# Optimization experiments

Measured on AMD Instinct MI355X. Metric: run time of the kernel, lower is better.

The kernel has to match this reference:

```python
import jax, jax.numpy as jnp
import numpy as np

T, D, N, H = 2032, 1408, 16, 88  # K == N (MHA vision attention)
BLOCK_SIZE = 128
ROPE_THETA = 10000.0


def _apply_rope_interleaved(x_tnh, freqs_cis):
    # x_tnh: [T, N, H]; freqs_cis: [T, H//2, 2] with (..., 0)=cos, (..., 1)=sin.
    cos = freqs_cis[:, None, :, 0]  # [T, 1, H//2]
    sin = freqs_cis[:, None, :, 1]
    x1 = x_tnh[..., 0::2]
    x2 = x_tnh[..., 1::2]
    # interleaved rotation: pairs (even, odd) rotated by angle theta_t
    rot = jnp.stack([x1 * cos - x2 * sin, x1 * sin + x2 * cos], axis=-1)
    return rot.reshape(x_tnh.shape)


def setup_inputs() -> dict:
    key = jax.random.key(0)
    ks = jax.random.split(key, 10)
    s = 0.02
    x = jax.random.normal(ks[0], (T, D), dtype=jnp.float32)
    # precomputed rotary cos/sin table (interleaved ordering)
    pos = jnp.arange(T, dtype=jnp.float32)
    inv_freq = ROPE_THETA ** (-jnp.arange(0, H, 2, dtype=jnp.float32) / H)  # [H//2]
    ang = pos[:, None] * inv_freq[None, :]                                  # [T, H//2]
    freqs_cis = jnp.stack([jnp.cos(ang), jnp.sin(ang)], axis=-1)            # [T, H//2, 2]
    Wq = jax.random.normal(ks[1], (D, N, H), dtype=jnp.float32) * s
    Wk = jax.random.normal(ks[2], (D, N, H), dtype=jnp.float32) * s
    Wv = jax.random.normal(ks[3], (D, N, H), dtype=jnp.float32) * s
    Wo = jax.random.normal(ks[4], (N, H, D), dtype=jnp.float32) * s
    bq = jax.random.normal(ks[5], (N, H), dtype=jnp.float32) * s
    bk = jax.random.normal(ks[6], (N, H), dtype=jnp.float32) * s
    bv = jax.random.normal(ks[7], (N, H), dtype=jnp.float32) * s
    bo = jax.random.normal(ks[8], (D,), dtype=jnp.float32) * s
    return {"x": x, "freqs_cis": freqs_cis, "Wq": Wq, "bq": bq, "Wk": Wk,
            "bk": bk, "Wv": Wv, "bv": bv, "Wo": Wo, "bo": bo}


def reference(x, freqs_cis, Wq, bq, Wk, bk, Wv, bv, Wo, bo):
    t, d = x.shape
    n, h = bq.shape
    sm_scale = h ** -0.5
    # fused QKV projections + bias + RoPE (q, k only)
    q = jnp.einsum('td,dnh->tnh', x, Wq) + bq[None]
    q = _apply_rope_interleaved(q, freqs_cis)
    k = jnp.einsum('td,dkh->tkh', x, Wk) + bk[None]
    k = _apply_rope_interleaved(k, freqs_cis)
    v = jnp.einsum('td,dkh->tkh', x, Wv) + bv[None]
    # pad T up to a multiple of BLOCK_SIZE, as the flash-attention call requires
    pad_len = (BLOCK_SIZE - t % BLOCK_SIZE) % BLOCK_SIZE
    qp = jnp.pad(q, ((0, pad_len), (0, 0), (0, 0)))
    kp = jnp.pad(k, ((0, pad_len), (0, 0), (0, 0)))
    vp = jnp.pad(v, ((0, pad_len), (0, 0), (0, 0)))
    # [N, Tp, H]
    qh = jnp.transpose(qp, (1, 0, 2))
    kh = jnp.transpose(kp, (1, 0, 2))
    vh = jnp.transpose(vp, (1, 0, 2))
    # segment ids: 0 for valid tokens, 1 for padding; attention only within equal ids
    seg = jnp.concatenate([jnp.zeros((t,), jnp.int32), jnp.ones((pad_len,), jnp.int32)])
    mask = seg[:, None] == seg[None, :]  # [Tp, Tp]
    scores = jnp.einsum('nth,nsh->nts', qh, kh) * sm_scale
    scores = jnp.where(mask[None], scores, jnp.finfo(scores.dtype).min)
    probs = jax.nn.softmax(scores, axis=-1)
    out = jnp.einsum('nts,nsh->nth', probs, vh)        # [N, Tp, H]
    out = jnp.transpose(out, (1, 0, 2))[:t]            # [T, N, H]
    o = jnp.einsum('tnh,nhd->td', out, Wo) + bo
    return o
```

## Files before the change

### kernel.cpp

```cpp
#include <hip/hip_runtime.h>
#include <hip/hip_bf16.h>
#include <stdint.h>
#include <stddef.h>

typedef __bf16 bf16_t;
typedef __bf16 bf16x8 __attribute__((ext_vector_type(8)));
typedef __bf16 bf16x4 __attribute__((ext_vector_type(4)));
typedef float  f32x4  __attribute__((ext_vector_type(4)));

#define T_SEQ 2032
#define T_PAD 2048
#define DM    1408
#define NHEAD 16
#define HD    88
#define HPQ   96
#define HPK   128
#define HPV   96
#define KVB   64
#define NT    (T_PAD / KVB)
#define SM_SCALE 0.10660035817780521f

__device__ __forceinline__ void gload_lds16(const bf16_t* g, bf16_t* l) {
  __builtin_amdgcn_global_load_lds(
      (__attribute__((address_space(1))) void*)(g),
      (__attribute__((address_space(3))) void*)(l), 16, 0, 0);
}

__global__ void k_convert_x(const float* __restrict__ x, bf16_t* __restrict__ Xb) {
  int idx = blockIdx.x * 256 + threadIdx.x;
  const int total = T_PAD * DM / 4;
  if (idx >= total) return;
  int base = idx * 4;
  int t = base / DM;
  float4 v;
  if (t < T_SEQ) v = *(const float4*)(x + base);
  else           v = make_float4(0.f, 0.f, 0.f, 0.f);
  bf16x4 o;
  o[0] = (bf16_t)v.x; o[1] = (bf16_t)v.y; o[2] = (bf16_t)v.z; o[3] = (bf16_t)v.w;
  *(bf16x4*)(Xb + base) = o;
}

__device__ __forceinline__ void transpose_body(const float* __restrict__ src,
                                               bf16_t* __restrict__ dst,
                                               int R, int C, int blk) {
  __shared__ float tile[32][33];
  const int tiles_c = C >> 5;
  const int tr = blk / tiles_c;
  const int tc = blk % tiles_c;
  const int lane = threadIdx.x & 31;
  const int row  = threadIdx.x >> 5;
#pragma unroll
  for (int i = 0; i < 32; i += 8)
    tile[row + i][lane] = src[(size_t)(tr * 32 + row + i) * C + tc * 32 + lane];
  __syncthreads();
#pragma unroll
  for (int i = 0; i < 32; i += 8)
    dst[(size_t)(tc * 32 + row + i) * R + tr * 32 + lane] = (bf16_t)tile[lane][row + i];
}

__global__ void k_transpose3(const float* __restrict__ Wq, const float* __restrict__ Wk,
                             const float* __restrict__ Wv, bf16_t* __restrict__ dst) {
  const int which = blockIdx.x / 1936;
  const int b = blockIdx.x % 1936;
  const float* src = (which == 0) ? Wq : (which == 1) ? Wk : Wv;
  transpose_body(src, dst + (size_t)which * DM * DM, DM, DM, b);
}

__global__ void k_transpose1(const float* __restrict__ src, bf16_t* __restrict__ dst) {
  transpose_body(src, dst, DM, DM, blockIdx.x);
}

__global__ void k_bias(const float* __restrict__ bq, const float* __restrict__ bk,
                       const float* __restrict__ bv, float* __restrict__ bias) {
  int i = blockIdx.x * 256 + threadIdx.x;
  if (i >= 3 * DM) return;
  bias[i] = (i < DM) ? bq[i] : ((i < 2 * DM) ? bk[i - DM] : bv[i - 2 * DM]);
}

__device__ __forceinline__ void gemm_main_1408(
    const bf16_t* __restrict__ A, const bf16_t* __restrict__ Bt,
    bf16_t* As, bf16_t* Bs, int m0, int n0, f32x4 acc[4][4]) {
  const int tid = threadIdx.x;
  const int w = tid >> 6, lane = tid & 63;
  const int l15 = lane & 15, lg = lane >> 4;
  const int b0 = w * 2048 + lane * 16;
  const int r0 = b0 >> 6, k0 = (b0 & 63) >> 1;
  const int b1 = b0 + 1024;
  const int r1 = b1 >> 6, k1 = (b1 & 63) >> 1;
  const int wr = w >> 1, wc = w & 1;
  const size_t aoff0 = (size_t)(m0 + r0) * DM + k0;
  const size_t aoff1 = (size_t)(m0 + r1) * DM + k1;
  const size_t boff0 = (size_t)(n0 + r0) * DM + k0;
  const size_t boff1 = (size_t)(n0 + r1) * DM + k1;
  for (int kt = 0; kt < 44; ++kt) {
    const int ko = kt * 32;
    gload_lds16(A + aoff0 + ko, As + w * 1024);
    gload_lds16(A + aoff1 + ko, As + w * 1024 + 512);
    gload_lds16(Bt + boff0 + ko, Bs + w * 1024);
    gload_lds16(Bt + boff1 + ko, Bs + w * 1024 + 512);
    __syncthreads();
    bf16x8 av[4], bv[4];
#pragma unroll
    for (int m = 0; m < 4; ++m)
      av[m] = *(const bf16x8*)(As + (wr * 64 + m * 16 + l15) * 32 + lg * 8);
#pragma unroll
    for (int n = 0; n < 4; ++n)
      bv[n] = *(const bf16x8*)(Bs + (wc * 64 + n * 16 + l15) * 32 + lg * 8);
#pragma unroll
    for (int m = 0; m < 4; ++m)
#pragma unroll
      for (int n = 0; n < 4; ++n)
        acc[m][n] = __builtin_amdgcn_mfma_f32_16x16x32_bf16(av[m], bv[n], acc[m][n], 0, 0, 0);
    __syncthreads();
  }
}

__global__ __launch_bounds__(256, 2) void k_gemm_qkv(
    const bf16_t* __restrict__ A, const bf16_t* __restrict__ Bt,
    const float* __restrict__ bias, const float* __restrict__ freqs,
    bf16_t* __restrict__ Qh, bf16_t* __restrict__ Kh, bf16_t* __restrict__ Vt) {
  __shared__ bf16_t As[128 * 32];
  __shared__ bf16_t Bs[128 * 32];
  const int bid = blockIdx.x;
  const int sbid = (bid & 7) * 66 + (bid >> 3);
  const int mt = sbid / 33, nt = sbid % 33;
  f32x4 acc[4][4];
#pragma unroll
  for (int m = 0; m < 4; ++m)
#pragma unroll
    for (int n = 0; n < 4; ++n) acc[m][n] = (f32x4){0.f, 0.f, 0.f, 0.f};
  gemm_main_1408(A, Bt, As, Bs, mt * 128, nt * 128, acc);
  const int tid = threadIdx.x, w = tid >> 6, lane = tid & 63;
  const int l15 = lane & 15, lg = lane >> 4;
  const int wr = w >> 1, wc = w & 1;
  const int cb = nt * 128 + wc * 64, rb = mt * 128 + wr * 64;
#pragma unroll
  for (int n = 0; n < 4; ++n) {
    const int col = cb + n * 16 + l15;
    const float bv = bias[col];
    const int seg = (col >= 2 * DM) ? 2 : ((col >= DM) ? 1 : 0);
    const int cc = col - seg * DM;
    const int hn = cc / 88;
    const int hh = cc - hn * 88;
    const int hbase = hh & ~1;
    const bool odd = hh & 1;
#pragma unroll
    for (int m = 0; m < 4; ++m) {
      const int tb = rb + m * 16 + lg * 4;
      if (seg == 2) {
        bf16x4 vv;
#pragma unroll
        for (int r = 0; r < 4; ++r) vv[r] = (bf16_t)(acc[m][n][r] + bv);
        *(bf16x4*)(Vt + ((size_t)hn * HPV + hh) * T_PAD + tb) = vv;
      } else {
#pragma unroll
        for (int r = 0; r < 4; ++r) {
          const int t = tb + r;
          const float v = acc[m][n][r] + bv;
          const float p = __shfl_xor(v, 1);
          const int tc2 = (t < T_SEQ) ? t : 0;
          const float c = freqs[tc2 * 88 + hbase];
          const float s = freqs[tc2 * 88 + hbase + 1];
          const float x1 = odd ? p : v;
          const float x2 = odd ? v : p;
          const float ro = odd ? (x1 * s + x2 * c) : (x1 * c - x2 * s);
          if (seg == 0)
            Qh[((size_t)hn * T_PAD + t) * HPQ + hh] = (bf16_t)(ro * SM_SCALE);
          else
            Kh[((size_t)hn * T_PAD + t) * HPK + hh] = (bf16_t)ro;
        }
      }
    }
  }
}

__global__ __launch_bounds__(256, 2) void k_gemm_out64(
    const bf16_t* __restrict__ A, const bf16_t* __restrict__ Bt,
    const float* __restrict__ bo, float* __restrict__ out) {
  __shared__ bf16_t Sm[6144];
  const int bid = blockIdx.x;
  const int sbid = (bid & 7) * 44 + (bid >> 3);
  const int mt = sbid / 11, nt = sbid % 11;
  const int m0 = mt * 64, n0 = nt * 128;
  const int tid = threadIdx.x, w = tid >> 6, lane = tid & 63;
  const int l15 = lane & 15, lg = lane >> 4;
  const bf16_t* srcp[3];
  size_t srco[3];
  int dste[3];
#pragma unroll
  for (int p = 0; p < 3; ++p) {
    const int off = w * 3072 + p * 1024;
    const int o = off + lane * 16;
    dste[p] = off >> 1;
    if (off < 4096) {
      int r = o >> 6, k = (o & 63) >> 1;
      srcp[p] = A; srco[p] = (size_t)(m0 + r) * DM + k;
    } else {
      int ob = o - 4096;
      int r = ob >> 6, k = (ob & 63) >> 1;
      srcp[p] = Bt; srco[p] = (size_t)(n0 + r) * DM + k;
    }
  }
  f32x4 acc[4][2];
#pragma unroll
  for (int m = 0; m < 4; ++m)
#pragma unroll
    for (int n = 0; n < 2; ++n) acc[m][n] = (f32x4){0.f, 0.f, 0.f, 0.f};
  for (int kt = 0; kt < 44; ++kt) {
    const int ko = kt * 32;
#pragma unroll
    for (int p = 0; p < 3; ++p)
      gload_lds16(srcp[p] + srco[p] + ko, Sm + dste[p]);
    __syncthreads();
    bf16x8 av[4], bv2[2];
#pragma unroll
    for (int m = 0; m < 4; ++m)
      av[m] = *(const bf16x8*)(Sm + (m * 16 + l15) * 32 + lg * 8);
#pragma unroll
    for (int n = 0; n < 2; ++n)
      bv2[n] = *(const bf16x8*)(Sm + 2048 + (w * 32 + n * 16 + l15) * 32 + lg * 8);
#pragma unroll
    for (int m = 0; m < 4; ++m)
#pragma unroll
      for (int n = 0; n < 2; ++n)
        acc[m][n] = __builtin_amdgcn_mfma_f32_16x16x32_bf16(av[m], bv2[n], acc[m][n], 0, 0, 0);
    __syncthreads();
  }
  const int cb = n0 + w * 32;
#pragma unroll
  for (int n = 0; n < 2; ++n) {
    const int col = cb + n * 16 + l15;
    const float bv = bo[col];
#pragma unroll
    for (int m = 0; m < 4; ++m) {
#pragma unroll
      for (int r = 0; r < 4; ++r) {
        const int t = m0 + m * 16 + lg * 4 + r;
        if (t < T_SEQ) out[(size_t)t * DM + col] = acc[m][n][r] + bv;
      }
    }
  }
}

__global__ __launch_bounds__(256, 3) void k_attn(
    const bf16_t* __restrict__ Qh, const bf16_t* __restrict__ Kh,
    const bf16_t* __restrict__ Vt, bf16_t* __restrict__ Ob) {
  __shared__ bf16_t Ks[2][KVB * 128];
  __shared__ bf16_t Vs[HPV * KVB];
  __shared__ bf16_t Ps[4][16 * 72];
  const int tid = threadIdx.x;
  const int w = tid >> 6, lane = tid & 63;
  const int l15 = lane & 15, lg = lane >> 4;
  const int swz = l15 & 7;
  const int bid = blockIdx.x;
  const int sbid = (bid & 7) * 64 + (bid >> 3);
  const int head = sbid >> 5;
  const int qt = sbid & 31;
  const bf16_t* Qn = Qh + (size_t)head * T_PAD * HPQ;
  const bf16_t* Kn = Kh + (size_t)head * T_PAD * HPK;
  const bf16_t* Vn = Vt + (size_t)head * HPV * T_PAD;
  const int q0 = qt * 64 + w * 16;

  bf16x8 qf[3];
#pragma unroll
  for (int kh = 0; kh < 3; ++kh)
    qf[kh] = *(const bf16x8*)(Qn + (size_t)(q0 + l15) * HPQ + kh * 32 + lg * 8);

  f32x4 oacc[6];
#pragma unroll
  for (int j = 0; j < 6; ++j) oacc[j] = (f32x4){0.f, 0.f, 0.f, 0.f};
  float mrow[4] = {-1e30f, -1e30f, -1e30f, -1e30f};
  float lrowp[4] = {0.f, 0.f, 0.f, 0.f};

  int kro[4], kco[4];
#pragma unroll
  for (int p = 0; p < 4; ++p) {
    int o = (w * 4 + p) * 1024 + lane * 16;
    int row = o >> 8, ch = (o >> 4) & 15;
    kro[p] = row; kco[p] = (ch ^ (row & 7)) << 3;
  }
  int vro[3], vco[3];
#pragma unroll
  for (int p = 0; p < 3; ++p) {
    int o = (w * 3 + p) * 1024 + lane * 16;
    int row = o >> 7, ch = (o >> 4) & 7;
    vro[p] = row; vco[p] = (ch ^ (row & 7)) << 3;
  }

#pragma unroll
  for (int p = 0; p < 4; ++p)
    gload_lds16(Kn + (size_t)kro[p] * HPK + kco[p], &Ks[0][(w * 4 + p) * 512]);
#pragma unroll
  for (int p = 0; p < 3; ++p)
    gload_lds16(Vn + (size_t)vro[p] * T_PAD + vco[p], &Vs[(w * 3 + p) * 512]);

  for (int kvt = 0; kvt < NT; ++kvt) {
    const int s0 = kvt * KVB;
    const int cur = kvt & 1;
    const int nxt = (kvt + 1 < NT) ? kvt + 1 : 0;
#pragma unroll
    for (int p = 0; p < 4; ++p)
      gload_lds16(Kn + (size_t)(nxt * KVB + kro[p]) * HPK + kco[p],
                  &Ks[cur ^ 1][(w * 4 + p) * 512]);
    asm volatile("s_waitcnt vmcnt(4)" ::: "memory");
    __builtin_amdgcn_s_barrier();

    const bf16_t* Kc = Ks[cur];
    f32x4 sf[4];
    __builtin_amdgcn_s_setprio(1);
#pragma unroll
    for (int ss = 0; ss < 4; ++ss) {
      const int rowK = ss * 16 + l15;
      f32x4 s = {0.f, 0.f, 0.f, 0.f};
#pragma unroll
      for (int kh = 0; kh < 3; ++kh) {
        bf16x8 kf = *(const bf16x8*)(Kc + rowK * 128 + (((kh * 4 + lg) ^ swz) << 3));
        s = __builtin_amdgcn_mfma_f32_16x16x32_bf16(qf[kh], kf, s, 0, 0, 0);
      }
      if (s0 + rowK >= T_SEQ) s = (f32x4){-1e30f, -1e30f, -1e30f, -1e30f};
      sf[ss] = s;
    }
    __builtin_amdgcn_s_setprio(0);
    float tm[4];
#pragma unroll
    for (int r = 0; r < 4; ++r)
      tm[r] = fmaxf(fmaxf(sf[0][r], sf[1][r]), fmaxf(sf[2][r], sf[3][r]));
#pragma unroll
    for (int d = 1; d < 16; d <<= 1)
#pragma unroll
      for (int r = 0; r < 4; ++r) tm[r] = fmaxf(tm[r], __shfl_xor(tm[r], d, 16));
    float sc[4];
#pragma unroll
    for (int r = 0; r < 4; ++r) {
      float mn = fmaxf(mrow[r], tm[r]);
      sc[r] = __expf(mrow[r] - mn);
      mrow[r] = mn;
    }
#pragma unroll
    for (int r = 0; r < 4; ++r) {
      float rs = 0.f;
#pragma unroll
      for (int ss = 0; ss < 4; ++ss) {
        float p = __expf(sf[ss][r] - mrow[r]);
        sf[ss][r] = p;
        rs += p;
      }
      lrowp[r] = lrowp[r] * sc[r] + rs;
    }
#pragma unroll
    for (int j = 0; j < 6; ++j)
#pragma unroll
      for (int r = 0; r < 4; ++r) oacc[j][r] *= sc[r];
#pragma unroll
    for (int ss = 0; ss < 4; ++ss)
#pragma unroll
      for (int r = 0; r < 4; ++r)
        Ps[w][(lg * 4 + r) * 72 + ss * 16 + l15] = (bf16_t)sf[ss][r];
    bf16x8 pa[2];
#pragma unroll
    for (int ks = 0; ks < 2; ++ks)
      pa[ks] = *(const bf16x8*)(&Ps[w][l15 * 72 + ks * 32 + lg * 8]);
    __builtin_amdgcn_s_setprio(1);
#pragma unroll
    for (int j = 0; j < 6; ++j)
#pragma unroll
      for (int ks = 0; ks < 2; ++ks) {
        bf16x8 vf = *(const bf16x8*)(Vs + (j * 16 + l15) * KVB + (((ks * 4 + lg) ^ swz) << 3));
        oacc[j] = __builtin_amdgcn_mfma_f32_16x16x32_bf16(pa[ks], vf, oacc[j], 0, 0, 0);
      }
    __builtin_amdgcn_s_setprio(0);
    __builtin_amdgcn_s_barrier();
#pragma unroll
    for (int p = 0; p < 3; ++p)
      gload_lds16(Vn + (size_t)vro[p] * T_PAD + nxt * KVB + vco[p],
                  &Vs[(w * 3 + p) * 512]);
  }
  asm volatile("s_waitcnt vmcnt(0)" ::: "memory");

#pragma unroll
  for (int d = 1; d < 16; d <<= 1)
#pragma unroll
    for (int r = 0; r < 4; ++r) lrowp[r] += __shfl_xor(lrowp[r], d, 16);

#pragma unroll
  for (int j = 0; j < 6; ++j) {
    const int h = j * 16 + l15;
    if (h < HD) {
#pragma unroll
      for (int r = 0; r < 4; ++r) {
        const int t = q0 + lg * 4 + r;
        if (t < T_SEQ)
          Ob[(size_t)t * DM + head * HD + h] = (bf16_t)(oacc[j][r] / lrowp[r]);
      }
    }
  }
}

extern "C" void kernel_launch(void* const* d_in, const int* in_sizes, int n_in,
                              void* d_out, int out_size, void* d_ws, size_t ws_size,
                              hipStream_t stream) {
  (void)in_sizes; (void)n_in; (void)out_size; (void)ws_size;
  const float* x     = (const float*)d_in[0];
  const float* freqs = (const float*)d_in[1];
  const float* Wq    = (const float*)d_in[2];
  const float* bq    = (const float*)d_in[3];
  const float* Wk    = (const float*)d_in[4];
  const float* bk    = (const float*)d_in[5];
  const float* Wv    = (const float*)d_in[6];
  const float* bv    = (const float*)d_in[7];
  const float* Wo    = (const float*)d_in[8];
  const float* bo    = (const float*)d_in[9];
  float* out = (float*)d_out;
  char* ws = (char*)d_ws;

  bf16_t* Xb   = (bf16_t*)(ws);
  bf16_t* Wt   = (bf16_t*)(ws + 5767168);
  float*  bias = (float*) (ws + 17661952);
  bf16_t* Qh   = (bf16_t*)(ws + 17678848);
  bf16_t* Kh   = (bf16_t*)(ws + 23970304);
  bf16_t* Vt   = (bf16_t*)(ws + 32358912);
  bf16_t* Ob   = Xb;
  bf16_t* Wot  = Wt;

  hipMemsetAsync(Qh, 0, 14680064, stream);

  k_convert_x<<<(T_PAD * DM / 4 + 255) / 256, 256, 0, stream>>>(x, Xb);
  k_transpose3<<<3 * 1936, 256, 0, stream>>>(Wq, Wk, Wv, Wt);
  k_bias<<<17, 256, 0, stream>>>(bq, bk, bv, bias);

  k_gemm_qkv<<<16 * 33, 256, 0, stream>>>(Xb, Wt, bias, freqs, Qh, Kh, Vt);

  k_transpose1<<<1936, 256, 0, stream>>>(Wo, Wot);

  k_attn<<<NHEAD * 32, 256, 0, stream>>>(Qh, Kh, Vt, Ob);
  k_gemm_out64<<<32 * 11, 256, 0, stream>>>(Ob, Wot, bo, out);
}
```

Before: 256.5 us.

## Double-buffer GEMMs, merge weight transposes, rework attention with deferred rescale

The three Wq/Wk/Wv transposes and the Wo transpose are merged into one kernel that uses 64x64 float4 tiles, and the separate bias-concat kernel is dropped. Both GEMMs now double-buffer their LDS tiles, prefetching the next K-slice before computing the current one and raising wave priority around the MFMAs. Attention is restructured: the score tile is computed transposed as K·Q with KV blocks of 128, and K/V are read straight from global memory instead of staged through LDS. Softmax uses exp2, with log2e folded into the Q scale, and skips the running-max rescale unless the max grows past a threshold. These changes add register pressure and move all K/V reuse onto the caches, and the Wo placement now depends on the workspace size.

```diff
diff --git a/kernel.cpp b/kernel.cpp
--- a/kernel.cpp
+++ b/kernel.cpp
@@ -13,12 +13,12 @@
 #define DM    1408
 #define NHEAD 16
 #define HD    88
-#define HPQ   96
-#define HPK   128
-#define HPV   96
-#define KVB   64
+#define HP    96
+#define KVB   128
 #define NT    (T_PAD / KVB)
 #define SM_SCALE 0.10660035817780521f
+#define LOG2E 1.4426950408889634f
+#define DEFER_THR 8.0f
 
 __device__ __forceinline__ void gload_lds16(const bf16_t* g, bf16_t* l) {
   __builtin_amdgcn_global_load_lds(
@@ -40,46 +40,38 @@
   *(bf16x4*)(Xb + base) = o;
 }
 
-__device__ __forceinline__ void transpose_body(const float* __restrict__ src,
-                                               bf16_t* __restrict__ dst,
-                                               int R, int C, int blk) {
-  __shared__ float tile[32][33];
-  const int tiles_c = C >> 5;
-  const int tr = blk / tiles_c;
-  const int tc = blk % tiles_c;
-  const int lane = threadIdx.x & 31;
-  const int row  = threadIdx.x >> 5;
-#pragma unroll
-  for (int i = 0; i < 32; i += 8)
-    tile[row + i][lane] = src[(size_t)(tr * 32 + row + i) * C + tc * 32 + lane];
+__global__ void k_transpose4(const float* __restrict__ W0, const float* __restrict__ W1,
+                             const float* __restrict__ W2, const float* __restrict__ W3,
+                             bf16_t* __restrict__ d012, bf16_t* __restrict__ d3) {
+  const int which = blockIdx.x / 484;
+  const int b = blockIdx.x % 484;
+  const float* src = (which == 0) ? W0 : (which == 1) ? W1 : (which == 2) ? W2 : W3;
+  bf16_t* dst = (which < 3) ? (d012 + (size_t)which * DM * DM) : d3;
+  const int tr = b / 22, tc = b % 22;
+  __shared__ float tile[64][65];
+  const int t = threadIdx.x;
+  const int row = t >> 2, l4 = t & 3;
+#pragma unroll
+  for (int i = 0; i < 4; ++i) {
+    float4 v = *(const float4*)(src + (size_t)(tr * 64 + row) * DM + tc * 64 + l4 * 16 + i * 4);
+    *(float4*)&tile[row][l4 * 16 + i * 4] = v;
+  }
   __syncthreads();
-#pragma unroll
-  for (int i = 0; i < 32; i += 8)
-    dst[(size_t)(tc * 32 + row + i) * R + tr * 32 + lane] = (bf16_t)tile[lane][row + i];
-}
-
-__global__ void k_transpose3(const float* __restrict__ Wq, const float* __restrict__ Wk,
-                             const float* __restrict__ Wv, bf16_t* __restrict__ dst) {
-  const int which = blockIdx.x / 1936;
-  const int b = blockIdx.x % 1936;
-  const float* src = (which == 0) ? Wq : (which == 1) ? Wk : Wv;
-  transpose_body(src, dst + (size_t)which * DM * DM, DM, DM, b);
-}
-
-__global__ void k_transpose1(const float* __restrict__ src, bf16_t* __restrict__ dst) {
-  transpose_body(src, dst, DM, DM, blockIdx.x);
-}
-
-__global__ void k_bias(const float* __restrict__ bq, const float* __restrict__ bk,
-                       const float* __restrict__ bv, float* __restrict__ bias) {
-  int i = blockIdx.x * 256 + threadIdx.x;
-  if (i >= 3 * DM) return;
-  bias[i] = (i < DM) ? bq[i] : ((i < 2 * DM) ? bk[i - DM] : bv[i - 2 * DM]);
+  const int jj = t >> 2;
+#pragma unroll
+  for (int it = 0; it < 2; ++it) {
+    const int c = (t & 3) + 4 * it;
+    bf16x8 o;
+#pragma unroll
+    for (int e = 0; e < 8; ++e) o[e] = (bf16_t)tile[c * 8 + e][jj];
+    *(bf16x8*)(dst + (size_t)(tc * 64 + jj) * DM + tr * 64 + c * 8) = o;
+  }
 }
 
 __device__ __forceinline__ void gemm_main_1408(
     const bf16_t* __restrict__ A, const bf16_t* __restrict__ Bt,
-    bf16_t* As, bf16_t* Bs, int m0, int n0, f32x4 acc[4][4]) {
+    bf16_t* As, bf16_t* Bs,
+    int m0, int n0, f32x4 acc[4][4]) {
   const int tid = threadIdx.x;
   const int w = tid >> 6, lane = tid & 63;
   const int l15 = lane & 15, lg = lane >> 4;
@@ -92,35 +84,48 @@
   const size_t aoff1 = (size_t)(m0 + r1) * DM + k1;
   const size_t boff0 = (size_t)(n0 + r0) * DM + k0;
   const size_t boff1 = (size_t)(n0 + r1) * DM + k1;
+  gload_lds16(A + aoff0, As + w * 1024);
+  gload_lds16(A + aoff1, As + w * 1024 + 512);
+  gload_lds16(Bt + boff0, Bs + w * 1024);
+  gload_lds16(Bt + boff1, Bs + w * 1024 + 512);
   for (int kt = 0; kt < 44; ++kt) {
-    const int ko = kt * 32;
-    gload_lds16(A + aoff0 + ko, As + w * 1024);
-    gload_lds16(A + aoff1 + ko, As + w * 1024 + 512);
-    gload_lds16(Bt + boff0 + ko, Bs + w * 1024);
-    gload_lds16(Bt + boff1 + ko, Bs + w * 1024 + 512);
-    __syncthreads();
+    const int cur = kt & 1;
+    const int kon = ((kt < 43) ? kt + 1 : 43) * 32;
+    const int db = (cur ^ 1) * 4096;
+    gload_lds16(A + aoff0 + kon, As + db + w * 1024);
+    gload_lds16(A + aoff1 + kon, As + db + w * 1024 + 512);
+    gload_lds16(Bt + boff0 + kon, Bs + db + w * 1024);
+    gload_lds16(Bt + boff1 + kon, Bs + db + w * 1024 + 512);
+    asm volatile("s_waitcnt vmcnt(4)" ::: "memory");
+    __builtin_amdgcn_s_barrier();
+    const bf16_t* Ac = As + cur * 4096;
+    const bf16_t* Bc = Bs + cur * 4096;
     bf16x8 av[4], bv[4];
 #pragma unroll
     for (int m = 0; m < 4; ++m)
-      av[m] = *(const bf16x8*)(As + (wr * 64 + m * 16 + l15) * 32 + lg * 8);
+      av[m] = *(const bf16x8*)(Ac + (wr * 64 + m * 16 + l15) * 32 + lg * 8);
 #pragma unroll
     for (int n = 0; n < 4; ++n)
-      bv[n] = *(const bf16x8*)(Bs + (wc * 64 + n * 16 + l15) * 32 + lg * 8);
+      bv[n] = *(const bf16x8*)(Bc + (wc * 64 + n * 16 + l15) * 32 + lg * 8);
+    __builtin_amdgcn_s_setprio(1);
 #pragma unroll
     for (int m = 0; m < 4; ++m)
 #pragma unroll
       for (int n = 0; n < 4; ++n)
         acc[m][n] = __builtin_amdgcn_mfma_f32_16x16x32_bf16(av[m], bv[n], acc[m][n], 0, 0, 0);
-    __syncthreads();
-  }
+    __builtin_amdgcn_s_setprio(0);
+    __builtin_amdgcn_s_barrier();
+  }
+  asm volatile("s_waitcnt vmcnt(0)" ::: "memory");
 }
 
 __global__ __launch_bounds__(256, 2) void k_gemm_qkv(
     const bf16_t* __restrict__ A, const bf16_t* __restrict__ Bt,
-    const float* __restrict__ bias, const float* __restrict__ freqs,
+    const float* __restrict__ bq, const float* __restrict__ bk,
+    const float* __restrict__ bvp, const float* __restrict__ freqs,
     bf16_t* __restrict__ Qh, bf16_t* __restrict__ Kh, bf16_t* __restrict__ Vt) {
-  __shared__ bf16_t As[128 * 32];
-  __shared__ bf16_t Bs[128 * 32];
+  __shared__ bf16_t As[2 * 4096];
+  __shared__ bf16_t Bs[2 * 4096];
   const int bid = blockIdx.x;
   const int sbid = (bid & 7) * 66 + (bid >> 3);
   const int mt = sbid / 33, nt = sbid % 33;
@@ -137,9 +142,10 @@
 #pragma unroll
   for (int n = 0; n < 4; ++n) {
     const int col = cb + n * 16 + l15;
-    const float bv = bias[col];
     const int seg = (col >= 2 * DM) ? 2 : ((col >= DM) ? 1 : 0);
     const int cc = col - seg * DM;
+    const float* bp = (seg == 0) ? bq : (seg == 1) ? bk : bvp;
+    const float bval = bp[cc];
     const int hn = cc / 88;
     const int hh = cc - hn * 88;
     const int hbase = hh & ~1;
@@ -150,13 +156,13 @@
       if (seg == 2) {
         bf16x4 vv;
 #pragma unroll
-        for (int r = 0; r < 4; ++r) vv[r] = (bf16_t)(acc[m][n][r] + bv);
-        *(bf16x4*)(Vt + ((size_t)hn * HPV + hh) * T_PAD + tb) = vv;
+        for (int r = 0; r < 4; ++r) vv[r] = (bf16_t)(acc[m][n][r] + bval);
+        *(bf16x4*)(Vt + ((size_t)hn * HP + hh) * T_PAD + tb) = vv;
       } else {
 #pragma unroll
         for (int r = 0; r < 4; ++r) {
           const int t = tb + r;
-          const float v = acc[m][n][r] + bv;
+          const float v = acc[m][n][r] + bval;
           const float p = __shfl_xor(v, 1);
           const int tc2 = (t < T_SEQ) ? t : 0;
           const float c = freqs[tc2 * 88 + hbase];
@@ -165,9 +171,9 @@
           const float x2 = odd ? v : p;
           const float ro = odd ? (x1 * s + x2 * c) : (x1 * c - x2 * s);
           if (seg == 0)
-            Qh[((size_t)hn * T_PAD + t) * HPQ + hh] = (bf16_t)(ro * SM_SCALE);
+            Qh[((size_t)hn * T_PAD + t) * HP + hh] = (bf16_t)(ro * (SM_SCALE * LOG2E));
           else
-            Kh[((size_t)hn * T_PAD + t) * HPK + hh] = (bf16_t)ro;
+            Kh[((size_t)hn * T_PAD + t) * HP + hh] = (bf16_t)ro;
         }
       }
     }
@@ -177,7 +183,7 @@
 __global__ __launch_bounds__(256, 2) void k_gemm_out64(
     const bf16_t* __restrict__ A, const bf16_t* __restrict__ Bt,
     const float* __restrict__ bo, float* __restrict__ out) {
-  __shared__ bf16_t Sm[6144];
+  __shared__ bf16_t Sm[2 * 6144];
   const int bid = blockIdx.x;
   const int sbid = (bid & 7) * 44 + (bid >> 3);
   const int mt = sbid / 11, nt = sbid % 11;
@@ -206,182 +212,173 @@
   for (int m = 0; m < 4; ++m)
 #pragma unroll
     for (int n = 0; n < 2; ++n) acc[m][n] = (f32x4){0.f, 0.f, 0.f, 0.f};
+#pragma unroll
+  for (int p = 0; p < 3; ++p) gload_lds16(srcp[p] + srco[p], Sm + dste[p]);
   for (int kt = 0; kt < 44; ++kt) {
-    const int ko = kt * 32;
+    const int cur = kt & 1;
+    const int kon = ((kt < 43) ? kt + 1 : 43) * 32;
+    const int db = (cur ^ 1) * 6144;
 #pragma unroll
     for (int p = 0; p < 3; ++p)
-      gload_lds16(srcp[p] + srco[p] + ko, Sm + dste[p]);
-    __syncthreads();
+      gload_lds16(srcp[p] + srco[p] + kon, Sm + db + dste[p]);
+    asm volatile("s_waitcnt vmcnt(3)" ::: "memory");
+    __builtin_amdgcn_s_barrier();
+    const bf16_t* Sc = Sm + cur * 6144;
     bf16x8 av[4], bv2[2];
 #pragma unroll
     for (int m = 0; m < 4; ++m)
-      av[m] = *(const bf16x8*)(Sm + (m * 16 + l15) * 32 + lg * 8);
+      av[m] = *(const bf16x8*)(Sc + (m * 16 + l15) * 32 + lg * 8);
 #pragma unroll
     for (int n = 0; n < 2; ++n)
-      bv2[n] = *(const bf16x8*)(Sm + 2048 + (w * 32 + n * 16 + l15) * 32 + lg * 8);
+      bv2[n] = *(const bf16x8*)(Sc + 2048 + (w * 32 + n * 16 + l15) * 32 + lg * 8);
+    __builtin_amdgcn_s_setprio(1);
 #pragma unroll
     for (int m = 0; m < 4; ++m)
 #pragma unroll
       for (int n = 0; n < 2; ++n)
         acc[m][n] = __builtin_amdgcn_mfma_f32_16x16x32_bf16(av[m], bv2[n], acc[m][n], 0, 0, 0);
-    __syncthreads();
-  }
+    __builtin_amdgcn_s_setprio(0);
+    __builtin_amdgcn_s_barrier();
+  }
+  asm volatile("s_waitcnt vmcnt(0)" ::: "memory");
   const int cb = n0 + w * 32;
 #pragma unroll
   for (int n = 0; n < 2; ++n) {
     const int col = cb + n * 16 + l15;
-    const float bv = bo[col];
+    const float bval = bo[col];
 #pragma unroll
     for (int m = 0; m < 4; ++m) {
 #pragma unroll
       for (int r = 0; r < 4; ++r) {
         const int t = m0 + m * 16 + lg * 4 + r;
-        if (t < T_SEQ) out[(size_t)t * DM + col] = acc[m][n][r] + bv;
-      }
-    }
-  }
-}
-
-__global__ __launch_bounds__(256, 3) void k_attn(
+        if (t < T_SEQ) out[(size_t)t * DM + col] = acc[m][n][r] + bval;
+      }
+    }
+  }
+}
+
+__global__ __launch_bounds__(256, 2) void k_attn(
     const bf16_t* __restrict__ Qh, const bf16_t* __restrict__ Kh,
     const bf16_t* __restrict__ Vt, bf16_t* __restrict__ Ob) {
-  __shared__ bf16_t Ks[2][KVB * 128];
-  __shared__ bf16_t Vs[HPV * KVB];
-  __shared__ bf16_t Ps[4][16 * 72];
+  __shared__ bf16_t Ps[4][16 * 136];
   const int tid = threadIdx.x;
   const int w = tid >> 6, lane = tid & 63;
   const int l15 = lane & 15, lg = lane >> 4;
-  const int swz = l15 & 7;
   const int bid = blockIdx.x;
   const int sbid = (bid & 7) * 64 + (bid >> 3);
   const int head = sbid >> 5;
   const int qt = sbid & 31;
-  const bf16_t* Qn = Qh + (size_t)head * T_PAD * HPQ;
-  const bf16_t* Kn = Kh + (size_t)head * T_PAD * HPK;
-  const bf16_t* Vn = Vt + (size_t)head * HPV * T_PAD;
+  const bf16_t* Qn = Qh + (size_t)head * T_PAD * HP;
+  const bf16_t* Kn = Kh + (size_t)head * T_PAD * HP;
+  const bf16_t* Vn = Vt + (size_t)head * HP * T_PAD;
   const int q0 = qt * 64 + w * 16;
 
   bf16x8 qf[3];
 #pragma unroll
   for (int kh = 0; kh < 3; ++kh)
-    qf[kh] = *(const bf16x8*)(Qn + (size_t)(q0 + l15) * HPQ + kh * 32 + lg * 8);
+    qf[kh] = *(const bf16x8*)(Qn + (size_t)(q0 + l15) * HP + kh * 32 + lg * 8);
 
   f32x4 oacc[6];
 #pragma unroll
   for (int j = 0; j < 6; ++j) oacc[j] = (f32x4){0.f, 0.f, 0.f, 0.f};
-  float mrow[4] = {-1e30f, -1e30f, -1e30f, -1e30f};
-  float lrowp[4] = {0.f, 0.f, 0.f, 0.f};
-
-  int kro[4], kco[4];
-#pragma unroll
-  for (int p = 0; p < 4; ++p) {
-    int o = (w * 4 + p) * 1024 + lane * 16;
-    int row = o >> 8, ch = (o >> 4) & 15;
-    kro[p] = row; kco[p] = (ch ^ (row & 7)) << 3;
-  }
-  int vro[3], vco[3];
-#pragma unroll
-  for (int p = 0; p < 3; ++p) {
-    int o = (w * 3 + p) * 1024 + lane * 16;
-    int row = o >> 7, ch = (o >> 4) & 7;
-    vro[p] = row; vco[p] = (ch ^ (row & 7)) << 3;
-  }
-
-#pragma unroll
-  for (int p = 0; p < 4; ++p)
-    gload_lds16(Kn + (size_t)kro[p] * HPK + kco[p], &Ks[0][(w * 4 + p) * 512]);
-#pragma unroll
-  for (int p = 0; p < 3; ++p)
-    gload_lds16(Vn + (size_t)vro[p] * T_PAD + vco[p], &Vs[(w * 3 + p) * 512]);
+  float mrow = -1e30f;
+  float lrowp = 0.f;
 
   for (int kvt = 0; kvt < NT; ++kvt) {
     const int s0 = kvt * KVB;
-    const int cur = kvt & 1;
-    const int nxt = (kvt + 1 < NT) ? kvt + 1 : 0;
-#pragma unroll
-    for (int p = 0; p < 4; ++p)
-      gload_lds16(Kn + (size_t)(nxt * KVB + kro[p]) * HPK + kco[p],
-                  &Ks[cur ^ 1][(w * 4 + p) * 512]);
-    asm volatile("s_waitcnt vmcnt(4)" ::: "memory");
-    __builtin_amdgcn_s_barrier();
-
-    const bf16_t* Kc = Ks[cur];
-    f32x4 sf[4];
+    f32x4 sf[8];
+#pragma unroll
+    for (int half = 0; half < 2; ++half) {
+      bf16x8 kf[12];
+#pragma unroll
+      for (int ss = 0; ss < 4; ++ss)
+#pragma unroll
+        for (int kh = 0; kh < 3; ++kh)
+          kf[ss * 3 + kh] = *(const bf16x8*)(
+              Kn + (size_t)(s0 + (half * 4 + ss) * 16 + l15) * HP + kh * 32 + lg * 8);
+      __builtin_amdgcn_s_setprio(1);
+#pragma unroll
+      for (int ss = 0; ss < 4; ++ss) {
+        f32x4 s = {0.f, 0.f, 0.f, 0.f};
+#pragma unroll
+        for (int kh = 0; kh < 3; ++kh)
+          s = __builtin_amdgcn_mfma_f32_16x16x32_bf16(kf[ss * 3 + kh], qf[kh], s, 0, 0, 0);
+        sf[half * 4 + ss] = s;
+      }
+      __builtin_amdgcn_s_setprio(0);
+    }
+    bf16x8 vfA[12];
+#pragma unroll
+    for (int ks = 0; ks < 2; ++ks)
+#pragma unroll
+      for (int j = 0; j < 6; ++j)
+        vfA[ks * 6 + j] = *(const bf16x8*)(
+            Vn + (size_t)(j * 16 + l15) * T_PAD + s0 + ks * 32 + lg * 8);
+    if (s0 + KVB > T_SEQ) {
+#pragma unroll
+      for (int ss = 0; ss < 8; ++ss)
+#pragma unroll
+        for (int r = 0; r < 4; ++r)
+          if (s0 + ss * 16 + lg * 4 + r >= T_SEQ) sf[ss][r] = -1e30f;
+    }
+    float tm = sf[0][0];
+#pragma unroll
+    for (int ss = 0; ss < 8; ++ss)
+#pragma unroll
+      for (int r = 0; r < 4; ++r) tm = fmaxf(tm, sf[ss][r]);
+    tm = fmaxf(tm, __shfl_xor(tm, 16));
+    tm = fmaxf(tm, __shfl_xor(tm, 32));
+    if (!__all(tm <= mrow + DEFER_THR)) {
+      const float mn = fmaxf(mrow, tm);
+      const float scv = __builtin_amdgcn_exp2f(mrow - mn);
+      mrow = mn;
+      lrowp *= scv;
+#pragma unroll
+      for (int r = 0; r < 4; ++r) {
+        const float sq = __shfl(scv, lg * 4 + r, 16);
+#pragma unroll
+        for (int j = 0; j < 6; ++j) oacc[j][r] *= sq;
+      }
+    }
+    float rs = 0.f;
+#pragma unroll
+    for (int ss = 0; ss < 8; ++ss)
+#pragma unroll
+      for (int r = 0; r < 4; ++r) {
+        const float p = __builtin_amdgcn_exp2f(sf[ss][r] - mrow);
+        rs += p;
+        Ps[w][l15 * 136 + ss * 16 + lg * 4 + r] = (bf16_t)p;
+      }
+    lrowp += rs;
+    bf16x8 vfB[12];
+#pragma unroll
+    for (int ks = 0; ks < 2; ++ks)
+#pragma unroll
+      for (int j = 0; j < 6; ++j)
+        vfB[ks * 6 + j] = *(const bf16x8*)(
+            Vn + (size_t)(j * 16 + l15) * T_PAD + s0 + (ks + 2) * 32 + lg * 8);
     __builtin_amdgcn_s_setprio(1);
 #pragma unroll
-    for (int ss = 0; ss < 4; ++ss) {
-      const int rowK = ss * 16 + l15;
-      f32x4 s = {0.f, 0.f, 0.f, 0.f};
-#pragma unroll
-      for (int kh = 0; kh < 3; ++kh) {
-        bf16x8 kf = *(const bf16x8*)(Kc + rowK * 128 + (((kh * 4 + lg) ^ swz) << 3));
-        s = __builtin_amdgcn_mfma_f32_16x16x32_bf16(qf[kh], kf, s, 0, 0, 0);
-      }
-      if (s0 + rowK >= T_SEQ) s = (f32x4){-1e30f, -1e30f, -1e30f, -1e30f};
-      sf[ss] = s;
+    for (int ks = 0; ks < 2; ++ks) {
+      bf16x8 pa = *(const bf16x8*)(&Ps[w][l15 * 136 + ks * 32 + lg * 8]);
+#pragma unroll
+      for (int j = 0; j < 6; ++j)
+        oacc[j] = __builtin_amdgcn_mfma_f32_16x16x32_bf16(pa, vfA[ks * 6 + j], oacc[j], 0, 0, 0);
+    }
+#pragma unroll
+    for (int ks = 0; ks < 2; ++ks) {
+      bf16x8 pa = *(const bf16x8*)(&Ps[w][l15 * 136 + (ks + 2) * 32 + lg * 8]);
+#pragma unroll
+      for (int j = 0; j < 6; ++j)
+        oacc[j] = __builtin_amdgcn_mfma_f32_16x16x32_bf16(pa, vfB[ks * 6 + j], oacc[j], 0, 0, 0);
     }
     __builtin_amdgcn_s_setprio(0);
-    float tm[4];
-#pragma unroll
-    for (int r = 0; r < 4; ++r)
-      tm[r] = fmaxf(fmaxf(sf[0][r], sf[1][r]), fmaxf(sf[2][r], sf[3][r]));
-#pragma unroll
-    for (int d = 1; d < 16; d <<= 1)
-#pragma unroll
-      for (int r = 0; r < 4; ++r) tm[r] = fmaxf(tm[r], __shfl_xor(tm[r], d, 16));
-    float sc[4];
-#pragma unroll
-    for (int r = 0; r < 4; ++r) {
-      float mn = fmaxf(mrow[r], tm[r]);
-      sc[r] = __expf(mrow[r] - mn);
-      mrow[r] = mn;
-    }
-#pragma unroll
-    for (int r = 0; r < 4; ++r) {
-      float rs = 0.f;
-#pragma unroll
-      for (int ss = 0; ss < 4; ++ss) {
-        float p = __expf(sf[ss][r] - mrow[r]);
-        sf[ss][r] = p;
-        rs += p;
-      }
-      lrowp[r] = lrowp[r] * sc[r] + rs;
-    }
-#pragma unroll
-    for (int j = 0; j < 6; ++j)
-#pragma unroll
-      for (int r = 0; r < 4; ++r) oacc[j][r] *= sc[r];
-#pragma unroll
-    for (int ss = 0; ss < 4; ++ss)
-#pragma unroll
-      for (int r = 0; r < 4; ++r)
-        Ps[w][(lg * 4 + r) * 72 + ss * 16 + l15] = (bf16_t)sf[ss][r];
-    bf16x8 pa[2];
-#pragma unroll
-    for (int ks = 0; ks < 2; ++ks)
-      pa[ks] = *(const bf16x8*)(&Ps[w][l15 * 72 + ks * 32 + lg * 8]);
-    __builtin_amdgcn_s_setprio(1);
-#pragma unroll
-    for (int j = 0; j < 6; ++j)
-#pragma unroll
-      for (int ks = 0; ks < 2; ++ks) {
-        bf16x8 vf = *(const bf16x8*)(Vs + (j * 16 + l15) * KVB + (((ks * 4 + lg) ^ swz) << 3));
-        oacc[j] = __builtin_amdgcn_mfma_f32_16x16x32_bf16(pa[ks], vf, oacc[j], 0, 0, 0);
-      }
-    __builtin_amdgcn_s_setprio(0);
-    __builtin_amdgcn_s_barrier();
-#pragma unroll
-    for (int p = 0; p < 3; ++p)
-      gload_lds16(Vn + (size_t)vro[p] * T_PAD + nxt * KVB + vco[p],
-                  &Vs[(w * 3 + p) * 512]);
-  }
-  asm volatile("s_waitcnt vmcnt(0)" ::: "memory");
-
-#pragma unroll
-  for (int d = 1; d < 16; d <<= 1)
-#pragma unroll
-    for (int r = 0; r < 4; ++r) lrowp[r] += __shfl_xor(lrowp[r], d, 16);
-
+  }
+  lrowp += __shfl_xor(lrowp, 16);
+  lrowp += __shfl_xor(lrowp, 32);
+  float lq[4];
+#pragma unroll
+  for (int r = 0; r < 4; ++r) lq[r] = __shfl(lrowp, lg * 4 + r, 16);
 #pragma unroll
   for (int j = 0; j < 6; ++j) {
     const int h = j * 16 + l15;
@@ -390,7 +387,7 @@
       for (int r = 0; r < 4; ++r) {
         const int t = q0 + lg * 4 + r;
         if (t < T_SEQ)
-          Ob[(size_t)t * DM + head * HD + h] = (bf16_t)(oacc[j][r] / lrowp[r]);
+          Ob[(size_t)t * DM + head * HD + h] = (bf16_t)(oacc[j][r] / lq[r]);
       }
     }
   }
@@ -399,7 +396,7 @@
 extern "C" void kernel_launch(void* const* d_in, const int* in_sizes, int n_in,
                               void* d_out, int out_size, void* d_ws, size_t ws_size,
                               hipStream_t stream) {
-  (void)in_sizes; (void)n_in; (void)out_size; (void)ws_size;
+  (void)in_sizes; (void)n_in; (void)out_size;
   const float* x     = (const float*)d_in[0];
   const float* freqs = (const float*)d_in[1];
   const float* Wq    = (const float*)d_in[2];
@@ -413,24 +410,29 @@
   float* out = (float*)d_out;
   char* ws = (char*)d_ws;
 
-  bf16_t* Xb   = (bf16_t*)(ws);
-  bf16_t* Wt   = (bf16_t*)(ws + 5767168);
-  float*  bias = (float*) (ws + 17661952);
-  bf16_t* Qh   = (bf16_t*)(ws + 17678848);
-  bf16_t* Kh   = (bf16_t*)(ws + 23970304);
-  bf16_t* Vt   = (bf16_t*)(ws + 32358912);
-  bf16_t* Ob   = Xb;
-  bf16_t* Wot  = Wt;
-
-  hipMemsetAsync(Qh, 0, 14680064, stream);
+  bf16_t* Xb  = (bf16_t*)(ws);
+  bf16_t* Wt  = (bf16_t*)(ws + 5767168);
+  bf16_t* Qh  = (bf16_t*)(ws + 17661952);
+  bf16_t* Kh  = (bf16_t*)(ws + 23953408);
+  bf16_t* Vt  = (bf16_t*)(ws + 30244864);
+  bf16_t* Ob  = Xb;
+  const size_t NEED_ALL = 36536320ull + 3964928ull;
+  const bool sep_wot = (ws_size >= NEED_ALL);
+  bf16_t* Wot = sep_wot ? (bf16_t*)(ws + 36536320) : Wt;
+
+  hipMemsetAsync(Qh, 0, 6291456, stream);
 
   k_convert_x<<<(T_PAD * DM / 4 + 255) / 256, 256, 0, stream>>>(x, Xb);
-  k_transpose3<<<3 * 1936, 256, 0, stream>>>(Wq, Wk, Wv, Wt);
-  k_bias<<<17, 256, 0, stream>>>(bq, bk, bv, bias);
-
-  k_gemm_qkv<<<16 * 33, 256, 0, stream>>>(Xb, Wt, bias, freqs, Qh, Kh, Vt);
-
-  k_transpose1<<<1936, 256, 0, stream>>>(Wo, Wot);
+  if (sep_wot) {
+    k_transpose4<<<4 * 484, 256, 0, stream>>>(Wq, Wk, Wv, Wo, Wt, Wot);
+  } else {
+    k_transpose4<<<3 * 484, 256, 0, stream>>>(Wq, Wk, Wv, Wo, Wt, Wot);
+  }
+
+  k_gemm_qkv<<<16 * 33, 256, 0, stream>>>(Xb, Wt, bq, bk, bv, freqs, Qh, Kh, Vt);
+
+  if (!sep_wot)
+    k_transpose4<<<484, 256, 0, stream>>>(Wo, Wo, Wo, Wo, Wot, Wot);
 
   k_attn<<<NHEAD * 32, 256, 0, stream>>>(Qh, Kh, Vt, Ob);
   k_gemm_out64<<<32 * 11, 256, 0, stream>>>(Ob, Wot, bo, out);
```

New measurement: 302.6 us. 18.0% more time.
